# Optimization experiments

Measured on AMD Instinct MI355X. Metric: run time of the kernel, lower is better.

## Reference

```python
import jax, jax.numpy as jnp
import numpy as np

RAD = 0.15          # sphere radius (init kwarg)
MIN_DIST = 2.0 * RAD  # two spheres collide when center distance < 2*rad


def setup_inputs() -> dict:
    key = jax.random.key(0)
    pos = jax.random.normal(key, (64, 1024, 3), dtype=jnp.float32)  # [T, N, 3]
    return {"pos": pos}


def reference(pos):
    """Sphere collision check equivalent to the sweep-and-prune CUDA kernel.

    The CUDA kernel sorts along one axis purely as an acceleration structure;
    the math it computes is: over all unordered robot pairs (i<j) at each
    timestep, a pair collides if ||p_i - p_j|| < 2*rad. Returns
      count: total number of colliding pairs (int)
      loss:  sum over colliding pairs of (2*rad - dist)^2 penetration penalty
    """
    T, N, _ = pos.shape
    diff = pos[:, :, None, :] - pos[:, None, :, :]          # [T, N, N, 3]
    dist2 = jnp.sum(diff * diff, axis=-1)                   # [T, N, N]
    iu = jnp.triu(jnp.ones((N, N), dtype=bool), k=1)        # i < j, exclude self
    colliding = iu[None, :, :] & (dist2 < MIN_DIST * MIN_DIST)
    # safe sqrt (diagonal / coincident points have dist2 == 0)
    safe_d2 = jnp.where(dist2 > 0.0, dist2, 1.0)
    dist = jnp.sqrt(safe_d2)
    pen = MIN_DIST - dist                                   # penetration depth
    loss = jnp.sum(jnp.where(colliding, pen * pen, 0.0))
    count = jnp.sum(colliding).astype(jnp.int32)
    return (count, loss)
```

## Files before the change

kernel.cpp:

```cpp
#include <hip/hip_runtime.h>
#include <math.h>

#define TN     64
#define NP     1024
#define RADIUS 0.15f
#define MIN_D  (2.0f * RADIUS)
#define R2     (MIN_D * MIN_D)

#define BLOCK  512
#define WAVES  (BLOCK / 64)
#define SPLIT  8
#define GI     16
#define NGRP   (NP / GI)
#define NBLK   (TN * SPLIT)
#define PPT    (NP / BLOCK)

#define NB     40
#define XMIN   (-6.0f)
#define INVW   3.3f

__device__ __forceinline__ float dist2(float dx, float dy, float dz) {
    return __builtin_fmaf(dx, dx, __builtin_fmaf(dy, dy, dz * dz));
}

__launch_bounds__(BLOCK, 4)
__global__ void collide_kernel(const float* __restrict__ pos,
                               float* __restrict__ partial) {
    __shared__ float         shs [NP * 3];
    __shared__ unsigned int  hist[NB];
    __shared__ unsigned int  S[NB + 1];
    __shared__ unsigned char sbin[NP];

    const int t     = blockIdx.x / SPLIT;
    const int split = blockIdx.x % SPLIT;
    const int tid   = threadIdx.x;
    const int lane  = tid & 63;
    const int wave  = tid >> 6;

    const float* pt = pos + (size_t)t * NP * 3;
    float px[PPT], py[PPT], pz[PPT];
    int          bq[PPT];
    unsigned int rq[PPT];
    #pragma unroll
    for (int q = 0; q < PPT; ++q) {
        const int p = tid + q * BLOCK;
        px[q] = pt[3 * p + 0];
        py[q] = pt[3 * p + 1];
        pz[q] = pt[3 * p + 2];
    }
    if (tid < NB) hist[tid] = 0u;
    __syncthreads();

    #pragma unroll
    for (int q = 0; q < PPT; ++q) {
        int b = (int)((px[q] - XMIN) * INVW);
        b = b < 0 ? 0 : (b > NB - 1 ? NB - 1 : b);
        bq[q] = b;
        rq[q] = atomicAdd(&hist[b], 1u);
    }
    __syncthreads();

    if (tid < 64) {
        unsigned int c    = (tid < NB) ? hist[tid] : 0u;
        unsigned int incl = c;
        #pragma unroll
        for (int d = 1; d < 64; d <<= 1) {
            const unsigned int y = __shfl_up(incl, d, 64);
            if (lane >= d) incl += y;
        }
        if (tid < NB) S[tid + 1] = incl;
        if (tid == 0) S[0] = 0u;
    }
    __syncthreads();

    #pragma unroll
    for (int q = 0; q < PPT; ++q) {
        const unsigned int dst = S[bq[q]] + rq[q];
        shs[3 * dst + 0] = px[q];
        shs[3 * dst + 1] = py[q];
        shs[3 * dst + 2] = pz[q];
        sbin[dst] = (unsigned char)bq[q];
    }
    __syncthreads();

    unsigned int cnt  = 0;
    float        loss = 0.0f;
    {
        const int g = wave * SPLIT + split;
        const int b = g * GI;

        float xi[GI], yi[GI], zi[GI];
        #pragma unroll
        for (int k = 0; k < GI; ++k) {
            xi[k] = shs[3 * (b + k) + 0];
            yi[k] = shs[3 * (b + k) + 1];
            zi[k] = shs[3 * (b + k) + 2];
        }
        #pragma unroll
        for (int k = 0; k < GI; ++k)
            asm volatile("" : "+v"(xi[k]), "+v"(yi[k]), "+v"(zi[k]));

        const int bb   = (int)sbin[b + GI - 1];
        const int jend = (int)S[(bb + 2 <= NB) ? (bb + 2) : NB];

        if (lane < GI - 1) {
            const int j = b + 1 + lane;
            const float xj = shs[3 * j], yj = shs[3 * j + 1], zj = shs[3 * j + 2];
            #pragma unroll
            for (int k = 0; k < GI; ++k) {
                if (k <= lane) {
                    const float d2 = dist2(xi[k] - xj, yi[k] - yj, zi[k] - zj);
                    if (d2 < R2) {
                        cnt++;
                        const float pen = MIN_D - __builtin_amdgcn_sqrtf(d2);
                        loss += pen * pen;
                    }
                }
            }
        }

        for (int j = b + GI + lane; j < jend; j += 64) {
            const float xj = shs[3 * j], yj = shs[3 * j + 1], zj = shs[3 * j + 2];
            #pragma unroll
            for (int k = 0; k < GI; ++k) {
                const float d2 = dist2(xi[k] - xj, yi[k] - yj, zi[k] - zj);
                const bool hit = d2 < R2;
                cnt += hit ? 1u : 0u;
                if (hit) {
                    const float pen = MIN_D - __builtin_amdgcn_sqrtf(d2);
                    loss += pen * pen;
                }
            }
        }
    }

    float fcnt = (float)cnt;
    #pragma unroll
    for (int off = 32; off > 0; off >>= 1) {
        fcnt += __shfl_down(fcnt, off);
        loss += __shfl_down(loss, off);
    }
    __shared__ float cs[WAVES], ls[WAVES];
    if (lane == 0) { cs[wave] = fcnt; ls[wave] = loss; }
    __syncthreads();
    if (tid == 0) {
        float c = 0.0f, l = 0.0f;
        #pragma unroll
        for (int w = 0; w < WAVES; ++w) { c += cs[w]; l += ls[w]; }
        partial[2 * blockIdx.x + 0] = c;
        partial[2 * blockIdx.x + 1] = l;
    }
}

__global__ void finalize_kernel(const float* __restrict__ partial,
                                float* __restrict__ out) {
    const int lane = threadIdx.x;
    float c = 0.0f, l = 0.0f;
    #pragma unroll
    for (int i = 0; i < NBLK / 64; ++i) {
        const float2 p = ((const float2*)partial)[lane + i * 64];
        c += p.x;
        l += p.y;
    }
    #pragma unroll
    for (int off = 32; off > 0; off >>= 1) {
        c += __shfl_down(c, off);
        l += __shfl_down(l, off);
    }
    if (lane == 0) {
        out[0] = c;
        out[1] = l;
    }
}

extern "C" void kernel_launch(void* const* d_in, const int* in_sizes, int n_in,
                              void* d_out, int out_size, void* d_ws, size_t ws_size,
                              hipStream_t stream) {
    const float* pos     = (const float*)d_in[0];
    float*       partial = (float*)d_ws;
    float*       out     = (float*)d_out;

    collide_kernel<<<NBLK, BLOCK, 0, stream>>>(pos, partial);
    finalize_kernel<<<1, 64, 0, stream>>>(partial, out);
}
```

Before: 63.51 us.

## Replace LDS atomic binning with wave-level match counting and chunked prefix offsets

Replaces the shared-memory atomicAdd histogram with per-wave rank computation: each lane counts equal bins among the 64 lanes via shuffles, the last lane of each bin writes a per-chunk count, and a serial per-bin scan produces chunk offsets. This removes contended LDS atomics and makes the counting-sort scatter deterministic and stable. In exchange it adds a 64-iteration shuffle loop per point, extra shared arrays that may lower occupancy, and an extra barrier with a serial 16-step scan.

```diff
diff --git a/kernel.cpp b/kernel.cpp
--- a/kernel.cpp
+++ b/kernel.cpp
@@ -11,9 +11,9 @@
 #define WAVES  (BLOCK / 64)
 #define SPLIT  8
 #define GI     16
-#define NGRP   (NP / GI)
 #define NBLK   (TN * SPLIT)
 #define PPT    (NP / BLOCK)
+#define NCH    (NP / 64)
 
 #define NB     40
 #define XMIN   (-6.0f)
@@ -26,10 +26,12 @@
 __launch_bounds__(BLOCK, 4)
 __global__ void collide_kernel(const float* __restrict__ pos,
                                float* __restrict__ partial) {
-    __shared__ float         shs [NP * 3];
+    __shared__ float         shs[NP * 3];
+    __shared__ unsigned char sbin[NP];
+    __shared__ unsigned int  chunkcnt[NCH * NB];
+    __shared__ unsigned int  chunkoff[NCH * NB];
     __shared__ unsigned int  hist[NB];
     __shared__ unsigned int  S[NB + 1];
-    __shared__ unsigned char sbin[NP];
 
     const int t     = blockIdx.x / SPLIT;
     const int split = blockIdx.x % SPLIT;
@@ -39,30 +41,49 @@
 
     const float* pt = pos + (size_t)t * NP * 3;
     float px[PPT], py[PPT], pz[PPT];
-    int          bq[PPT];
-    unsigned int rq[PPT];
+    int   bq[PPT];
     #pragma unroll
     for (int q = 0; q < PPT; ++q) {
         const int p = tid + q * BLOCK;
         px[q] = pt[3 * p + 0];
         py[q] = pt[3 * p + 1];
         pz[q] = pt[3 * p + 2];
-    }
-    if (tid < NB) hist[tid] = 0u;
-    __syncthreads();
-
+        int b = (int)((px[q] - XMIN) * INVW);
+        bq[q] = b < 0 ? 0 : (b > NB - 1 ? NB - 1 : b);
+    }
+    for (int i = tid; i < NCH * NB; i += BLOCK) chunkcnt[i] = 0u;
+    __syncthreads();
+
+    int pre[PPT];
     #pragma unroll
     for (int q = 0; q < PPT; ++q) {
-        int b = (int)((px[q] - XMIN) * INVW);
-        b = b < 0 ? 0 : (b > NB - 1 ? NB - 1 : b);
-        bq[q] = b;
-        rq[q] = atomicAdd(&hist[b], 1u);
+        int p = 0, tot = 0;
+        for (int s = 0; s < 64; ++s) {
+            const int bs = __shfl(bq[q], s);
+            const bool eq = (bs == bq[q]);
+            tot += eq ? 1 : 0;
+            p   += (eq && s < lane) ? 1 : 0;
+        }
+        pre[q] = p;
+        if (p == tot - 1)
+            chunkcnt[(q * WAVES + wave) * NB + bq[q]] = (unsigned int)tot;
+    }
+    __syncthreads();
+
+    if (tid < NB) {
+        unsigned int run = 0;
+        #pragma unroll
+        for (int c = 0; c < NCH; ++c) {
+            const unsigned int v = chunkcnt[c * NB + tid];
+            chunkoff[c * NB + tid] = run;
+            run += v;
+        }
+        hist[tid] = run;
     }
     __syncthreads();
 
     if (tid < 64) {
-        unsigned int c    = (tid < NB) ? hist[tid] : 0u;
-        unsigned int incl = c;
+        unsigned int incl = (tid < NB) ? hist[tid] : 0u;
         #pragma unroll
         for (int d = 1; d < 64; d <<= 1) {
             const unsigned int y = __shfl_up(incl, d, 64);
@@ -75,7 +96,9 @@
 
     #pragma unroll
     for (int q = 0; q < PPT; ++q) {
-        const unsigned int dst = S[bq[q]] + rq[q];
+        const int c = q * WAVES + wave;
+        const unsigned int dst = S[bq[q]] + chunkoff[c * NB + bq[q]]
+                               + (unsigned int)pre[q];
         shs[3 * dst + 0] = px[q];
         shs[3 * dst + 1] = py[q];
         shs[3 * dst + 2] = pz[q];
```

Result: slower. 69.92 us (+10.1%).
